# Performance work log

Measured on AMD Instinct MI355X. Metric: run time of the kernel, lower is better.

Reference implementation:

```python
import jax, jax.numpy as jnp
import numpy as np

KH = KW = 9
STRIDE = 1
PAD = 4
DIL = 1


def _bilinear(img, py, px):
    """img: [C,H,W]; py, px: [kk,Ho,Wo] float sample coords -> [C,kk,Ho,Wo].
    Zero padding outside the image, matching DCNv2 semantics."""
    H, W = img.shape[-2], img.shape[-1]
    y0 = jnp.floor(py)
    x0 = jnp.floor(px)
    wy = py - y0  # fractional parts (carry the gradient wrt offsets)
    wx = px - x0

    def gather(yi, xi):
        valid = ((yi >= 0) & (yi < H) & (xi >= 0) & (xi < W)).astype(img.dtype)
        yc = jnp.clip(yi, 0, H - 1).astype(jnp.int32)
        xc = jnp.clip(xi, 0, W - 1).astype(jnp.int32)
        return img[:, yc, xc] * valid[None]

    v00 = gather(y0, x0)
    v01 = gather(y0, x0 + 1)
    v10 = gather(y0 + 1, x0)
    v11 = gather(y0 + 1, x0 + 1)
    return (v00 * (1 - wy) * (1 - wx) + v01 * (1 - wy) * wx
            + v10 * wy * (1 - wx) + v11 * wy * wx)


def setup_inputs() -> dict:
    key = jax.random.key(0)
    k1, k2, k3 = jax.random.split(key, 3)
    B, H, W = 2, 256, 256
    kk = KH * KW
    inp = jax.random.normal(k1, (B, 3, H, W), dtype=jnp.float32)
    offset = jax.random.normal(k2, (B, 2 * kk, H, W), dtype=jnp.float32)
    mask = jax.random.uniform(k3, (B, kk, H, W), dtype=jnp.float32)
    weight = jnp.ones((1, 1, KH, KW), dtype=jnp.float32) / kk  # frozen averaging kernel
    bias = jnp.zeros((1,), dtype=jnp.float32)
    return {"input": inp, "offset": offset, "mask": mask, "weight": weight, "bias": bias}


def reference(input, offset, mask, weight, bias):
    B, C, H, W = input.shape  # C = 3 * Ci (R,G,B chunks sharing weight/offset/mask)
    kk = KH * KW
    Ho = (H + 2 * PAD - DIL * (KH - 1) - 1) // STRIDE + 1
    Wo = (W + 2 * PAD - DIL * (KW - 1) - 1) // STRIDE + 1

    ky = jnp.repeat(jnp.arange(KH), KW)  # [kk]
    kx = jnp.tile(jnp.arange(KW), KH)
    base_y = (jnp.arange(Ho) * STRIDE - PAD)[None, :, None] + (ky * DIL)[:, None, None]  # [kk,Ho,1]
    base_x = (jnp.arange(Wo) * STRIDE - PAD)[None, None, :] + (kx * DIL)[:, None, None]  # [kk,1,Wo]

    off = offset.reshape(B, kk, 2, Ho, Wo)  # channel c = 2*k + {0: dy, 1: dx}
    py = base_y[None].astype(offset.dtype) + off[:, :, 0]  # [B,kk,Ho,Wo]
    px = base_x[None].astype(offset.dtype) + off[:, :, 1]

    # bilinear-sampled, modulated im2col: [B, C, kk, Ho, Wo]
    samples = jax.vmap(_bilinear)(input, py, px)
    val = samples * mask[:, None]

    Co, Ci = weight.shape[0], weight.shape[1]
    G = C // Ci  # 3 color groups, identical weight applied to each
    val = val.reshape(B, G, Ci, kk, Ho, Wo)
    wk = weight.reshape(Co, Ci, kk)
    out = jnp.einsum('bgckhw,ock->bgohw', val, wk) + bias[None, None, :, None, None]
    return out.reshape(B, G * Co, Ho, Wo)
```

## Files before the change

### kernel.cpp

```cpp
#include <hip/hip_runtime.h>
#include <hip/hip_fp16.h>

#define HH 256
#define WW 256
#define KK 81
#define PLANE (HH * WW)
#define SLK 10
#define TR 21
#define TC 150
#define TAB (TR * TC)

__global__ __launch_bounds__(256) void pack_kernel(const float* __restrict__ in,
                                                   ushort4* __restrict__ img) {
    int idx = blockIdx.x * 256 + threadIdx.x;
    int b = idx >> 16;
    int pix = idx & 0xFFFF;
    const float* base = in + (size_t)b * 3 * PLANE + pix;
    _Float16 h0 = (_Float16)base[0];
    _Float16 h1 = (_Float16)base[PLANE];
    _Float16 h2 = (_Float16)base[2 * PLANE];
    ushort4 u;
    u.x = __builtin_bit_cast(unsigned short, h0);
    u.y = __builtin_bit_cast(unsigned short, h1);
    u.z = __builtin_bit_cast(unsigned short, h2);
    u.w = 0;
    img[idx] = u;
}

__device__ __forceinline__ void acc3(float w, unsigned int pa, unsigned int pb,
                                     float& ax, float& ay, float& az) {
    __half2 ha = __builtin_bit_cast(__half2, pa);
    __half2 hb = __builtin_bit_cast(__half2, pb);
    ax = fmaf(w, __low2float(ha), ax);
    ay = fmaf(w, __high2float(ha), ay);
    az = fmaf(w, __low2float(hb), az);
}

__global__ __launch_bounds__(128, 3) void dcn_kernel(
    const ushort4* __restrict__ img,
    const float* __restrict__ offset,
    const float* __restrict__ mask,
    const float* __restrict__ weight,
    const float* __restrict__ bias,
    float* __restrict__ out) {
    __shared__ uint2 tile[TAB];

    const int t = threadIdx.x;
    const int b = blockIdx.y;
    const int ho = blockIdx.x >> 1;
    const int xo = (blockIdx.x & 1) * 128;
    const int yb = ho - SLK;
    const ushort4* ib = img + (size_t)b * PLANE;

    for (int i = 0; i < 25; ++i) {
        int cid = t + i * 128;
        if (cid < TAB) {
            int r = cid / TC;
            int c = cid - r * TC;
            int iy = yb + r;
            int ix = xo - SLK + c;
            unsigned int pa = 0, pb = 0;
            if (((unsigned)iy < (unsigned)HH) & ((unsigned)ix < (unsigned)WW)) {
                ushort4 u = ib[iy * WW + ix];
                pa = (unsigned int)u.x | ((unsigned int)u.y << 16);
                pb = (unsigned int)u.z;
            }
            tile[cid] = make_uint2(pa, pb);
        }
    }
    __syncthreads();

    const float* orow = offset + (size_t)b * 2 * KK * PLANE + (size_t)ho * WW + xo;
    const float* mrow = mask + (size_t)b * KK * PLANE + (size_t)ho * WW + xo;

    const float wof = (float)t;
    float ax = 0.f, ay = 0.f, az = 0.f;
    bool escaped = false;

    for (int ky = 0; ky < 9; ++ky) {
        const int rshift = ky + (SLK - 4);
#pragma unroll
        for (int kxi = 0; kxi < 9; ++kxi) {
            const int k = ky * 9 + kxi;
            float dy = orow[(size_t)(2 * k) * PLANE + t];
            float dx = orow[(size_t)(2 * k + 1) * PLANE + t];
            float m = mrow[(size_t)k * PLANE + t];
            float wk = weight[k];

            float yf = floorf(dy);
            float wy = dy - yf;
            int r0 = (int)yf + rshift;

            float px = dx + wof;
            float xf = floorf(px);
            float wx = px - xf;
            int c0 = (int)xf + (kxi + (SLK - 4));

            bool ok = ((unsigned)r0 < (unsigned)(TR - 1)) &
                      ((unsigned)c0 < (unsigned)(TC - 1));
            escaped |= !ok;
            float mw = (ok ? m : 0.f) * wk;

            float w1y = wy * mw, w0y = mw - w1y;
            float u1 = 1.f - wx;
            float w00 = w0y * u1, w01 = w0y * wx;
            float w10 = w1y * u1, w11 = w1y * wx;

            int r0c = min(max(r0, 0), TR - 2);
            int c0c = min(max(c0, 0), TC - 2);
            const uint2* p = &tile[r0c * TC + c0c];
            uint2 q00 = p[0];
            uint2 q01 = p[1];
            uint2 q10 = p[TC];
            uint2 q11 = p[TC + 1];

            acc3(w00, q00.x, q00.y, ax, ay, az);
            acc3(w01, q01.x, q01.y, ax, ay, az);
            acc3(w10, q10.x, q10.y, ax, ay, az);
            acc3(w11, q11.x, q11.y, ax, ay, az);
        }
    }

    if (__builtin_expect(escaped, 0)) {
#pragma unroll 1
        for (int k = 0; k < KK; ++k) {
            int ky = k / 9;
            int kxi = k - ky * 9;
            float dy = orow[(size_t)(2 * k) * PLANE + t];
            float dx = orow[(size_t)(2 * k + 1) * PLANE + t];
            float m = mrow[(size_t)k * PLANE + t];

            float yf = floorf(dy);
            int r0 = (int)yf + ky + (SLK - 4);
            float px = dx + wof;
            float xf = floorf(px);
            int c0 = (int)xf + kxi + (SLK - 4);
            bool ok = ((unsigned)r0 < (unsigned)(TR - 1)) &
                      ((unsigned)c0 < (unsigned)(TC - 1));
            if (ok) continue;

            float wy = dy - yf;
            float wx = px - xf;
            int y0 = (int)yf + ho - 4 + ky;
            int x0 = (int)xf + xo + kxi - 4;
            int y1 = y0 + 1, x1 = x0 + 1;
            float mw = m * weight[k];
            float va0 = ((unsigned)y0 < (unsigned)HH) ? 1.f : 0.f;
            float va1 = ((unsigned)y1 < (unsigned)HH) ? 1.f : 0.f;
            float vb0 = ((unsigned)x0 < (unsigned)WW) ? 1.f : 0.f;
            float vb1 = ((unsigned)x1 < (unsigned)WW) ? 1.f : 0.f;
            float w1y = wy * mw, w0y = mw - w1y;
            float w00 = w0y * (1.f - wx) * va0 * vb0;
            float w01 = w0y * wx * va0 * vb1;
            float w10 = w1y * (1.f - wx) * va1 * vb0;
            float w11 = w1y * wx * va1 * vb1;
            int y0c = min(max(y0, 0), HH - 1);
            int y1c = min(max(y1, 0), HH - 1);
            int x0c = min(max(x0, 0), WW - 1);
            int x1c = min(max(x1, 0), WW - 1);
            ushort4 g00 = ib[y0c * WW + x0c];
            ushort4 g01 = ib[y0c * WW + x1c];
            ushort4 g10 = ib[y1c * WW + x0c];
            ushort4 g11 = ib[y1c * WW + x1c];
            acc3(w00, (unsigned int)g00.x | ((unsigned int)g00.y << 16), g00.z, ax, ay, az);
            acc3(w01, (unsigned int)g01.x | ((unsigned int)g01.y << 16), g01.z, ax, ay, az);
            acc3(w10, (unsigned int)g10.x | ((unsigned int)g10.y << 16), g10.z, ax, ay, az);
            acc3(w11, (unsigned int)g11.x | ((unsigned int)g11.y << 16), g11.z, ax, ay, az);
        }
    }

    float bs = bias[0];
    float* ob = out + (size_t)b * 3 * PLANE + (size_t)ho * WW + xo + t;
    ob[0] = ax + bs;
    ob[PLANE] = ay + bs;
    ob[2 * PLANE] = az + bs;
}

extern "C" void kernel_launch(void* const* d_in, const int* in_sizes, int n_in,
                              void* d_out, int out_size, void* d_ws, size_t ws_size,
                              hipStream_t stream) {
    const float* input = (const float*)d_in[0];
    const float* offset = (const float*)d_in[1];
    const float* mask = (const float*)d_in[2];
    const float* weight = (const float*)d_in[3];
    const float* bias = (const float*)d_in[4];
    float* out = (float*)d_out;

    const int B = in_sizes[0] / (3 * PLANE);
    ushort4* img = (ushort4*)d_ws;

    pack_kernel<<<B * PLANE / 256, 256, 0, stream>>>(input, img);
    dim3 grid(HH * 2, B);
    dcn_kernel<<<grid, 128, 0, stream>>>(img, offset, mask, weight, bias, out);
}
```

Before: 172.8 us.

## Stream offset/mask rows into LDS ring via async global_load_lds prefetch

Result: slower. 192.7 us (+11.5%).

```diff
diff --git a/kernel.cpp b/kernel.cpp
--- a/kernel.cpp
+++ b/kernel.cpp
@@ -9,6 +9,7 @@
 #define TR 21
 #define TC 150
 #define TAB (TR * TC)
+#define RD 8
 
 __global__ __launch_bounds__(256) void pack_kernel(const float* __restrict__ in,
                                                    ushort4* __restrict__ img) {
@@ -36,7 +37,14 @@
     az = fmaf(w, __low2float(hb), az);
 }
 
-__global__ __launch_bounds__(128, 3) void dcn_kernel(
+__device__ __forceinline__ void gload_lds4(const float* g, float* l) {
+    __builtin_amdgcn_global_load_lds(
+        (const __attribute__((address_space(1))) unsigned int*)g,
+        (__attribute__((address_space(3))) unsigned int*)l,
+        4, 0, 0);
+}
+
+__global__ __launch_bounds__(128, 2) void dcn_kernel(
     const ushort4* __restrict__ img,
     const float* __restrict__ offset,
     const float* __restrict__ mask,
@@ -44,13 +52,30 @@
     const float* __restrict__ bias,
     float* __restrict__ out) {
     __shared__ uint2 tile[TAB];
+    __shared__ float ring[2][RD][192];
+    __shared__ float wk[KK];
 
     const int t = threadIdx.x;
+    const int wv = t >> 6;
+    const int l = t & 63;
     const int b = blockIdx.y;
     const int ho = blockIdx.x >> 1;
     const int xo = (blockIdx.x & 1) * 128;
     const int yb = ho - SLK;
     const ushort4* ib = img + (size_t)b * PLANE;
+
+    if (t < KK) wk[t] = weight[t];
+
+    const float* orow = offset + (size_t)b * 2 * KK * PLANE + (size_t)ho * WW + xo + wv * 64;
+    const float* mrow = mask + (size_t)b * KK * PLANE + (size_t)ho * WW + xo + wv * 64;
+
+#pragma unroll
+    for (int j = 0; j < RD; ++j) {
+        float* slot = &ring[wv][j][0];
+        gload_lds4(orow + (size_t)(2 * j) * PLANE + l, slot);
+        gload_lds4(orow + (size_t)(2 * j + 1) * PLANE + l, slot + 64);
+        gload_lds4(mrow + (size_t)j * PLANE + l, slot + 128);
+    }
 
     for (int i = 0; i < 25; ++i) {
         int cid = t + i * 128;
@@ -70,55 +95,109 @@
     }
     __syncthreads();
 
-    const float* orow = offset + (size_t)b * 2 * KK * PLANE + (size_t)ho * WW + xo;
-    const float* mrow = mask + (size_t)b * KK * PLANE + (size_t)ho * WW + xo;
-
     const float wof = (float)t;
     float ax = 0.f, ay = 0.f, az = 0.f;
     bool escaped = false;
 
-    for (int ky = 0; ky < 9; ++ky) {
-        const int rshift = ky + (SLK - 4);
-#pragma unroll
-        for (int kxi = 0; kxi < 9; ++kxi) {
-            const int k = ky * 9 + kxi;
-            float dy = orow[(size_t)(2 * k) * PLANE + t];
-            float dx = orow[(size_t)(2 * k + 1) * PLANE + t];
-            float m = mrow[(size_t)k * PLANE + t];
-            float wk = weight[k];
-
-            float yf = floorf(dy);
-            float wy = dy - yf;
-            int r0 = (int)yf + rshift;
-
-            float px = dx + wof;
-            float xf = floorf(px);
-            float wx = px - xf;
-            int c0 = (int)xf + (kxi + (SLK - 4));
-
-            bool ok = ((unsigned)r0 < (unsigned)(TR - 1)) &
-                      ((unsigned)c0 < (unsigned)(TC - 1));
-            escaped |= !ok;
-            float mw = (ok ? m : 0.f) * wk;
-
-            float w1y = wy * mw, w0y = mw - w1y;
-            float u1 = 1.f - wx;
-            float w00 = w0y * u1, w01 = w0y * wx;
-            float w10 = w1y * u1, w11 = w1y * wx;
-
-            int r0c = min(max(r0, 0), TR - 2);
-            int c0c = min(max(c0, 0), TC - 2);
-            const uint2* p = &tile[r0c * TC + c0c];
-            uint2 q00 = p[0];
-            uint2 q01 = p[1];
-            uint2 q10 = p[TC];
-            uint2 q11 = p[TC + 1];
-
-            acc3(w00, q00.x, q00.y, ax, ay, az);
-            acc3(w01, q01.x, q01.y, ax, ay, az);
-            acc3(w10, q10.x, q10.y, ax, ay, az);
-            acc3(w11, q11.x, q11.y, ax, ay, az);
+#pragma unroll 1
+    for (int j = 0; j < 73; ++j) {
+        asm volatile("s_waitcnt vmcnt(21)" ::: "memory");
+        __builtin_amdgcn_sched_barrier(0);
+
+        const float* slot = &ring[wv][j & (RD - 1)][0];
+        float dy = slot[l];
+        float dx = slot[64 + l];
+        float m = slot[128 + l];
+        float wkv = wk[j];
+        asm volatile("s_waitcnt lgkmcnt(0)" ::: "memory");
+        __builtin_amdgcn_sched_barrier(0);
+
+        {
+            float* ns = &ring[wv][j & (RD - 1)][0];
+            gload_lds4(orow + (size_t)(2 * (j + RD)) * PLANE + l, ns);
+            gload_lds4(orow + (size_t)(2 * (j + RD) + 1) * PLANE + l, ns + 64);
+            gload_lds4(mrow + (size_t)(j + RD) * PLANE + l, ns + 128);
         }
+
+        const int ky = j / 9;
+        const int kxi = j - ky * 9;
+
+        float yf = floorf(dy);
+        float wy = dy - yf;
+        int r0 = (int)yf + ky + (SLK - 4);
+
+        float px = dx + wof;
+        float xf = floorf(px);
+        float wx = px - xf;
+        int c0 = (int)xf + kxi + (SLK - 4);
+
+        bool ok = ((unsigned)r0 < (unsigned)(TR - 1)) &
+                  ((unsigned)c0 < (unsigned)(TC - 1));
+        escaped |= !ok;
+        float mw = (ok ? m : 0.f) * wkv;
+
+        float w1y = wy * mw, w0y = mw - w1y;
+        float u1 = 1.f - wx;
+        float w00 = w0y * u1, w01 = w0y * wx;
+        float w10 = w1y * u1, w11 = w1y * wx;
+
+        int r0c = min(max(r0, 0), TR - 2);
+        int c0c = min(max(c0, 0), TC - 2);
+        const uint2* p = &tile[r0c * TC + c0c];
+        uint2 q00 = p[0];
+        uint2 q01 = p[1];
+        uint2 q10 = p[TC];
+        uint2 q11 = p[TC + 1];
+
+        acc3(w00, q00.x, q00.y, ax, ay, az);
+        acc3(w01, q01.x, q01.y, ax, ay, az);
+        acc3(w10, q10.x, q10.y, ax, ay, az);
+        acc3(w11, q11.x, q11.y, ax, ay, az);
+    }
+
+    asm volatile("s_waitcnt vmcnt(0)" ::: "memory");
+    __builtin_amdgcn_sched_barrier(0);
+#pragma unroll 1
+    for (int j = 73; j < KK; ++j) {
+        const float* slot = &ring[wv][j & (RD - 1)][0];
+        float dy = slot[l];
+        float dx = slot[64 + l];
+        float m = slot[128 + l];
+        float wkv = wk[j];
+
+        const int ky = j / 9;
+        const int kxi = j - ky * 9;
+
+        float yf = floorf(dy);
+        float wy = dy - yf;
+        int r0 = (int)yf + ky + (SLK - 4);
+        float px = dx + wof;
+        float xf = floorf(px);
+        float wx = px - xf;
+        int c0 = (int)xf + kxi + (SLK - 4);
+
+        bool ok = ((unsigned)r0 < (unsigned)(TR - 1)) &
+                  ((unsigned)c0 < (unsigned)(TC - 1));
+        escaped |= !ok;
+        float mw = (ok ? m : 0.f) * wkv;
+
+        float w1y = wy * mw, w0y = mw - w1y;
+        float u1 = 1.f - wx;
+        float w00 = w0y * u1, w01 = w0y * wx;
+        float w10 = w1y * u1, w11 = w1y * wx;
+
+        int r0c = min(max(r0, 0), TR - 2);
+        int c0c = min(max(c0, 0), TC - 2);
+        const uint2* p = &tile[r0c * TC + c0c];
+        uint2 q00 = p[0];
+        uint2 q01 = p[1];
+        uint2 q10 = p[TC];
+        uint2 q11 = p[TC + 1];
+
+        acc3(w00, q00.x, q00.y, ax, ay, az);
+        acc3(w01, q01.x, q01.y, ax, ay, az);
+        acc3(w10, q10.x, q10.y, ax, ay, az);
+        acc3(w11, q11.x, q11.y, ax, ay, az);
     }
 
     if (__builtin_expect(escaped, 0)) {
@@ -126,9 +205,9 @@
         for (int k = 0; k < KK; ++k) {
             int ky = k / 9;
             int kxi = k - ky * 9;
-            float dy = orow[(size_t)(2 * k) * PLANE + t];
-            float dx = orow[(size_t)(2 * k + 1) * PLANE + t];
-            float m = mrow[(size_t)k * PLANE + t];
+            float dy = orow[(size_t)(2 * k) * PLANE + l];
+            float dx = orow[(size_t)(2 * k + 1) * PLANE + l];
+            float m = mrow[(size_t)k * PLANE + l];
 
             float yf = floorf(dy);
             int r0 = (int)yf + ky + (SLK - 4);
@@ -144,7 +223,7 @@
             int y0 = (int)yf + ho - 4 + ky;
             int x0 = (int)xf + xo + kxi - 4;
             int y1 = y0 + 1, x1 = x0 + 1;
-            float mw = m * weight[k];
+            float mw = m * wk[k];
             float va0 = ((unsigned)y0 < (unsigned)HH) ? 1.f : 0.f;
             float va1 = ((unsigned)y1 < (unsigned)HH) ? 1.f : 0.f;
             float vb0 = ((unsigned)x0 < (unsigned)WW) ? 1.f : 0.f;
```

## Replace LDS tile with direct global gathers and split taps across waves

Applied to the files above, without the earlier changes.

After: 193.6 us. 1.12x slower.

```diff
diff --git a/kernel.cpp b/kernel.cpp
--- a/kernel.cpp
+++ b/kernel.cpp
@@ -5,10 +5,6 @@
 #define WW 256
 #define KK 81
 #define PLANE (HH * WW)
-#define SLK 10
-#define TR 21
-#define TC 150
-#define TAB (TR * TC)
 
 __global__ __launch_bounds__(256) void pack_kernel(const float* __restrict__ in,
                                                    ushort4* __restrict__ img) {
@@ -36,144 +32,101 @@
     az = fmaf(w, __low2float(hb), az);
 }
 
-__global__ __launch_bounds__(128, 3) void dcn_kernel(
+__global__ __launch_bounds__(128, 4) void dcn_kernel(
     const ushort4* __restrict__ img,
     const float* __restrict__ offset,
     const float* __restrict__ mask,
     const float* __restrict__ weight,
     const float* __restrict__ bias,
     float* __restrict__ out) {
-    __shared__ uint2 tile[TAB];
+    __shared__ float red[3][64];
 
     const int t = threadIdx.x;
+    const int wv = t >> 6;
+    const int l = t & 63;
+    const int bx = blockIdx.x;
     const int b = blockIdx.y;
-    const int ho = blockIdx.x >> 1;
-    const int xo = (blockIdx.x & 1) * 128;
-    const int yb = ho - SLK;
-    const ushort4* ib = img + (size_t)b * PLANE;
+    const int ho = bx >> 2;
+    const int xo = (bx & 3) * 64;
+    const uint2* ibq = (const uint2*)img + (size_t)b * PLANE;
 
-    for (int i = 0; i < 25; ++i) {
-        int cid = t + i * 128;
-        if (cid < TAB) {
-            int r = cid / TC;
-            int c = cid - r * TC;
-            int iy = yb + r;
-            int ix = xo - SLK + c;
-            unsigned int pa = 0, pb = 0;
-            if (((unsigned)iy < (unsigned)HH) & ((unsigned)ix < (unsigned)WW)) {
-                ushort4 u = ib[iy * WW + ix];
-                pa = (unsigned int)u.x | ((unsigned int)u.y << 16);
-                pb = (unsigned int)u.z;
-            }
-            tile[cid] = make_uint2(pa, pb);
-        }
-    }
-    __syncthreads();
+    const int kb = wv * 41;
+    const int nk = 41 - wv;
 
-    const float* orow = offset + (size_t)b * 2 * KK * PLANE + (size_t)ho * WW + xo;
-    const float* mrow = mask + (size_t)b * KK * PLANE + (size_t)ho * WW + xo;
+    const float* orow = offset + (size_t)b * 2 * KK * PLANE + (size_t)(2 * kb) * PLANE
+                        + (size_t)ho * WW + xo;
+    const float* mrow = mask + (size_t)b * KK * PLANE + (size_t)kb * PLANE
+                        + (size_t)ho * WW + xo;
 
-    const float wof = (float)t;
+    const int wo = xo + l;
     float ax = 0.f, ay = 0.f, az = 0.f;
-    bool escaped = false;
 
-    for (int ky = 0; ky < 9; ++ky) {
-        const int rshift = ky + (SLK - 4);
-#pragma unroll
-        for (int kxi = 0; kxi < 9; ++kxi) {
-            const int k = ky * 9 + kxi;
-            float dy = orow[(size_t)(2 * k) * PLANE + t];
-            float dx = orow[(size_t)(2 * k + 1) * PLANE + t];
-            float m = mrow[(size_t)k * PLANE + t];
-            float wk = weight[k];
+    int ky = (kb == 41) ? 4 : 0;
+    int kxi = (kb == 41) ? 5 : 0;
 
-            float yf = floorf(dy);
-            float wy = dy - yf;
-            int r0 = (int)yf + rshift;
+#pragma unroll 4
+    for (int j = 0; j < nk; ++j) {
+        const int k = kb + j;
+        float dy = orow[(size_t)(2 * j) * PLANE + l];
+        float dx = orow[(size_t)(2 * j + 1) * PLANE + l];
+        float m = mrow[(size_t)j * PLANE + l];
+        float wkv = weight[k];
 
-            float px = dx + wof;
-            float xf = floorf(px);
-            float wx = px - xf;
-            int c0 = (int)xf + (kxi + (SLK - 4));
+        float yf = floorf(dy);
+        float wy = dy - yf;
+        int y0 = (int)yf + (ho - 4 + ky);
+        float fx = dx + (float)(kxi - 4);
+        float xf = floorf(fx);
+        float wx = fx - xf;
+        int x0 = (int)xf + wo;
+        int y1 = y0 + 1, x1 = x0 + 1;
 
-            bool ok = ((unsigned)r0 < (unsigned)(TR - 1)) &
-                      ((unsigned)c0 < (unsigned)(TC - 1));
-            escaped |= !ok;
-            float mw = (ok ? m : 0.f) * wk;
+        float va0 = ((unsigned)y0 < (unsigned)HH) ? 1.f : 0.f;
+        float va1 = ((unsigned)y1 < (unsigned)HH) ? 1.f : 0.f;
+        float vb0 = ((unsigned)x0 < (unsigned)WW) ? 1.f : 0.f;
+        float vb1 = ((unsigned)x1 < (unsigned)WW) ? 1.f : 0.f;
+        int y0c = min(max(y0, 0), HH - 1);
+        int y1c = min(max(y1, 0), HH - 1);
+        int x0c = min(max(x0, 0), WW - 1);
+        int x1c = min(max(x1, 0), WW - 1);
 
-            float w1y = wy * mw, w0y = mw - w1y;
-            float u1 = 1.f - wx;
-            float w00 = w0y * u1, w01 = w0y * wx;
-            float w10 = w1y * u1, w11 = w1y * wx;
+        float mw = m * wkv;
+        float w1y = wy * mw, w0y = mw - w1y;
+        float u1 = 1.f - wx;
+        float w00 = w0y * u1 * va0 * vb0;
+        float w01 = w0y * wx * va0 * vb1;
+        float w10 = w1y * u1 * va1 * vb0;
+        float w11 = w1y * wx * va1 * vb1;
 
-            int r0c = min(max(r0, 0), TR - 2);
-            int c0c = min(max(c0, 0), TC - 2);
-            const uint2* p = &tile[r0c * TC + c0c];
-            uint2 q00 = p[0];
-            uint2 q01 = p[1];
-            uint2 q10 = p[TC];
-            uint2 q11 = p[TC + 1];
+        uint2 q00 = ibq[y0c * WW + x0c];
+        uint2 q01 = ibq[y0c * WW + x1c];
+        uint2 q10 = ibq[y1c * WW + x0c];
+        uint2 q11 = ibq[y1c * WW + x1c];
 
-            acc3(w00, q00.x, q00.y, ax, ay, az);
-            acc3(w01, q01.x, q01.y, ax, ay, az);
-            acc3(w10, q10.x, q10.y, ax, ay, az);
-            acc3(w11, q11.x, q11.y, ax, ay, az);
+        acc3(w00, q00.x, q00.y, ax, ay, az);
+        acc3(w01, q01.x, q01.y, ax, ay, az);
+        acc3(w10, q10.x, q10.y, ax, ay, az);
+        acc3(w11, q11.x, q11.y, ax, ay, az);
+
+        if (++kxi == 9) {
+            kxi = 0;
+            ++ky;
         }
     }
 
-    if (__builtin_expect(escaped, 0)) {
-#pragma unroll 1
-        for (int k = 0; k < KK; ++k) {
-            int ky = k / 9;
-            int kxi = k - ky * 9;
-            float dy = orow[(size_t)(2 * k) * PLANE + t];
-            float dx = orow[(size_t)(2 * k + 1) * PLANE + t];
-            float m = mrow[(size_t)k * PLANE + t];
-
-            float yf = floorf(dy);
-            int r0 = (int)yf + ky + (SLK - 4);
-            float px = dx + wof;
-            float xf = floorf(px);
-            int c0 = (int)xf + kxi + (SLK - 4);
-            bool ok = ((unsigned)r0 < (unsigned)(TR - 1)) &
-                      ((unsigned)c0 < (unsigned)(TC - 1));
-            if (ok) continue;
-
-            float wy = dy - yf;
-            float wx = px - xf;
-            int y0 = (int)yf + ho - 4 + ky;
-            int x0 = (int)xf + xo + kxi - 4;
-            int y1 = y0 + 1, x1 = x0 + 1;
-            float mw = m * weight[k];
-            float va0 = ((unsigned)y0 < (unsigned)HH) ? 1.f : 0.f;
-            float va1 = ((unsigned)y1 < (unsigned)HH) ? 1.f : 0.f;
-            float vb0 = ((unsigned)x0 < (unsigned)WW) ? 1.f : 0.f;
-            float vb1 = ((unsigned)x1 < (unsigned)WW) ? 1.f : 0.f;
-            float w1y = wy * mw, w0y = mw - w1y;
-            float w00 = w0y * (1.f - wx) * va0 * vb0;
-            float w01 = w0y * wx * va0 * vb1;
-            float w10 = w1y * (1.f - wx) * va1 * vb0;
-            float w11 = w1y * wx * va1 * vb1;
-            int y0c = min(max(y0, 0), HH - 1);
-            int y1c = min(max(y1, 0), HH - 1);
-            int x0c = min(max(x0, 0), WW - 1);
-            int x1c = min(max(x1, 0), WW - 1);
-            ushort4 g00 = ib[y0c * WW + x0c];
-            ushort4 g01 = ib[y0c * WW + x1c];
-            ushort4 g10 = ib[y1c * WW + x0c];
-            ushort4 g11 = ib[y1c * WW + x1c];
-            acc3(w00, (unsigned int)g00.x | ((unsigned int)g00.y << 16), g00.z, ax, ay, az);
-            acc3(w01, (unsigned int)g01.x | ((unsigned int)g01.y << 16), g01.z, ax, ay, az);
-            acc3(w10, (unsigned int)g10.x | ((unsigned int)g10.y << 16), g10.z, ax, ay, az);
-            acc3(w11, (unsigned int)g11.x | ((unsigned int)g11.y << 16), g11.z, ax, ay, az);
-        }
+    if (wv == 1) {
+        red[0][l] = ax;
+        red[1][l] = ay;
+        red[2][l] = az;
     }
-
-    float bs = bias[0];
-    float* ob = out + (size_t)b * 3 * PLANE + (size_t)ho * WW + xo + t;
-    ob[0] = ax + bs;
-    ob[PLANE] = ay + bs;
-    ob[2 * PLANE] = az + bs;
+    __syncthreads();
+    if (wv == 0) {
+        float bs = bias[0];
+        float* ob = out + (size_t)b * 3 * PLANE + (size_t)ho * WW + xo + l;
+        ob[0] = ax + red[0][l] + bs;
+        ob[PLANE] = ay + red[1][l] + bs;
+        ob[2 * PLANE] = az + red[2][l] + bs;
+    }
 }
 
 extern "C" void kernel_launch(void* const* d_in, const int* in_sizes, int n_in,
@@ -190,6 +143,6 @@
     ushort4* img = (ushort4*)d_ws;
 
     pack_kernel<<<B * PLANE / 256, 256, 0, stream>>>(input, img);
-    dim3 grid(HH * 2, B);
+    dim3 grid(HH * 4, B);
     dcn_kernel<<<grid, 128, 0, stream>>>(img, offset, mask, weight, bias, out);
 }
```

## Split kernel taps across waves with 4 pixels per lane and LDS reduction

Applied to the files above, without the earlier changes.

After: 171.5 us. No clear change (-0.8%).

```diff
diff --git a/kernel.cpp b/kernel.cpp
--- a/kernel.cpp
+++ b/kernel.cpp
@@ -7,8 +7,8 @@
 #define PLANE (HH * WW)
 #define SLK 10
 #define TR 21
-#define TC 150
-#define TAB (TR * TC)
+#define TCW 276
+#define TABW (TR * TCW)
 
 __global__ __launch_bounds__(256) void pack_kernel(const float* __restrict__ in,
                                                    ushort4* __restrict__ img) {
@@ -36,29 +36,31 @@
     az = fmaf(w, __low2float(hb), az);
 }
 
-__global__ __launch_bounds__(128, 3) void dcn_kernel(
+__global__ __launch_bounds__(256) void dcn_kernel(
     const ushort4* __restrict__ img,
     const float* __restrict__ offset,
     const float* __restrict__ mask,
     const float* __restrict__ weight,
     const float* __restrict__ bias,
     float* __restrict__ out) {
-    __shared__ uint2 tile[TAB];
+    __shared__ uint2 tile[TABW];
+    __shared__ float red[3][4][256];
 
     const int t = threadIdx.x;
+    const int w = t >> 6;
+    const int l = t & 63;
     const int b = blockIdx.y;
-    const int ho = blockIdx.x >> 1;
-    const int xo = (blockIdx.x & 1) * 128;
+    const int ho = blockIdx.x;
     const int yb = ho - SLK;
     const ushort4* ib = img + (size_t)b * PLANE;
 
-    for (int i = 0; i < 25; ++i) {
-        int cid = t + i * 128;
-        if (cid < TAB) {
-            int r = cid / TC;
-            int c = cid - r * TC;
+    for (int i = 0; i < 23; ++i) {
+        int cid = t + i * 256;
+        if (cid < TABW) {
+            int r = cid / TCW;
+            int c = cid - r * TCW;
             int iy = yb + r;
-            int ix = xo - SLK + c;
+            int ix = c - SLK;
             unsigned int pa = 0, pb = 0;
             if (((unsigned)iy < (unsigned)HH) & ((unsigned)ix < (unsigned)WW)) {
                 ushort4 u = ib[iy * WW + ix];
@@ -70,36 +72,49 @@
     }
     __syncthreads();
 
-    const float* orow = offset + (size_t)b * 2 * KK * PLANE + (size_t)ho * WW + xo;
-    const float* mrow = mask + (size_t)b * KK * PLANE + (size_t)ho * WW + xo;
-
-    const float wof = (float)t;
-    float ax = 0.f, ay = 0.f, az = 0.f;
-    bool escaped = false;
-
-    for (int ky = 0; ky < 9; ++ky) {
-        const int rshift = ky + (SLK - 4);
+    const int kbeg = w * 20 + (w ? 1 : 0);
+    const int nk = w ? 20 : 21;
+    int ky = kbeg / 9;
+    int kxi = kbeg - ky * 9;
+
+    const float* obase = offset + (size_t)b * 2 * KK * PLANE
+                         + (size_t)(2 * kbeg) * PLANE + (size_t)ho * WW;
+    const float* mbase = mask + (size_t)b * KK * PLANE
+                         + (size_t)kbeg * PLANE + (size_t)ho * WW;
+
+    float ax[4] = {0.f, 0.f, 0.f, 0.f};
+    float ay[4] = {0.f, 0.f, 0.f, 0.f};
+    float az[4] = {0.f, 0.f, 0.f, 0.f};
+    bool esc = false;
+
+#pragma unroll 2
+    for (int j = 0; j < nk; ++j) {
+        float4 dy4 = *(const float4*)(obase + (size_t)(2 * j) * PLANE + 4 * l);
+        float4 dx4 = *(const float4*)(obase + (size_t)(2 * j + 1) * PLANE + 4 * l);
+        float4 m4 = *(const float4*)(mbase + (size_t)j * PLANE + 4 * l);
+        float wkv = weight[kbeg + j];
+
+        const float dyv[4] = {dy4.x, dy4.y, dy4.z, dy4.w};
+        const float dxv[4] = {dx4.x, dx4.y, dx4.z, dx4.w};
+        const float mv[4] = {m4.x, m4.y, m4.z, m4.w};
+
 #pragma unroll
-        for (int kxi = 0; kxi < 9; ++kxi) {
-            const int k = ky * 9 + kxi;
-            float dy = orow[(size_t)(2 * k) * PLANE + t];
-            float dx = orow[(size_t)(2 * k + 1) * PLANE + t];
-            float m = mrow[(size_t)k * PLANE + t];
-            float wk = weight[k];
-
+        for (int i = 0; i < 4; ++i) {
+            const int wo = 4 * l + i;
+            float dy = dyv[i];
             float yf = floorf(dy);
             float wy = dy - yf;
-            int r0 = (int)yf + rshift;
-
-            float px = dx + wof;
-            float xf = floorf(px);
-            float wx = px - xf;
-            int c0 = (int)xf + (kxi + (SLK - 4));
+            int r0 = (int)yf + ky + (SLK - 4);
+
+            float fx = dxv[i] + (float)(kxi - 4);
+            float xf = floorf(fx);
+            float wx = fx - xf;
+            int c0 = (int)xf + wo + SLK;
 
             bool ok = ((unsigned)r0 < (unsigned)(TR - 1)) &
-                      ((unsigned)c0 < (unsigned)(TC - 1));
-            escaped |= !ok;
-            float mw = (ok ? m : 0.f) * wk;
+                      ((unsigned)c0 < (unsigned)(TCW - 1));
+            esc |= !ok;
+            float mw = (ok ? mv[i] : 0.f) * wkv;
 
             float w1y = wy * mw, w0y = mw - w1y;
             float u1 = 1.f - wx;
@@ -107,73 +122,100 @@
             float w10 = w1y * u1, w11 = w1y * wx;
 
             int r0c = min(max(r0, 0), TR - 2);
-            int c0c = min(max(c0, 0), TC - 2);
-            const uint2* p = &tile[r0c * TC + c0c];
+            int c0c = min(max(c0, 0), TCW - 2);
+            const uint2* p = &tile[r0c * TCW + c0c];
             uint2 q00 = p[0];
             uint2 q01 = p[1];
-            uint2 q10 = p[TC];
-            uint2 q11 = p[TC + 1];
-
-            acc3(w00, q00.x, q00.y, ax, ay, az);
-            acc3(w01, q01.x, q01.y, ax, ay, az);
-            acc3(w10, q10.x, q10.y, ax, ay, az);
-            acc3(w11, q11.x, q11.y, ax, ay, az);
-        }
-    }
-
-    if (__builtin_expect(escaped, 0)) {
+            uint2 q10 = p[TCW];
+            uint2 q11 = p[TCW + 1];
+
+            acc3(w00, q00.x, q00.y, ax[i], ay[i], az[i]);
+            acc3(w01, q01.x, q01.y, ax[i], ay[i], az[i]);
+            acc3(w10, q10.x, q10.y, ax[i], ay[i], az[i]);
+            acc3(w11, q11.x, q11.y, ax[i], ay[i], az[i]);
+        }
+
+        if (++kxi == 9) {
+            kxi = 0;
+            ++ky;
+        }
+    }
+
+    if (__builtin_expect(esc, 0)) {
 #pragma unroll 1
-        for (int k = 0; k < KK; ++k) {
-            int ky = k / 9;
-            int kxi = k - ky * 9;
-            float dy = orow[(size_t)(2 * k) * PLANE + t];
-            float dx = orow[(size_t)(2 * k + 1) * PLANE + t];
-            float m = mrow[(size_t)k * PLANE + t];
-
-            float yf = floorf(dy);
-            int r0 = (int)yf + ky + (SLK - 4);
-            float px = dx + wof;
-            float xf = floorf(px);
-            int c0 = (int)xf + kxi + (SLK - 4);
-            bool ok = ((unsigned)r0 < (unsigned)(TR - 1)) &
-                      ((unsigned)c0 < (unsigned)(TC - 1));
-            if (ok) continue;
-
-            float wy = dy - yf;
-            float wx = px - xf;
-            int y0 = (int)yf + ho - 4 + ky;
-            int x0 = (int)xf + xo + kxi - 4;
-            int y1 = y0 + 1, x1 = x0 + 1;
-            float mw = m * weight[k];
-            float va0 = ((unsigned)y0 < (unsigned)HH) ? 1.f : 0.f;
-            float va1 = ((unsigned)y1 < (unsigned)HH) ? 1.f : 0.f;
-            float vb0 = ((unsigned)x0 < (unsigned)WW) ? 1.f : 0.f;
-            float vb1 = ((unsigned)x1 < (unsigned)WW) ? 1.f : 0.f;
-            float w1y = wy * mw, w0y = mw - w1y;
-            float w00 = w0y * (1.f - wx) * va0 * vb0;
-            float w01 = w0y * wx * va0 * vb1;
-            float w10 = w1y * (1.f - wx) * va1 * vb0;
-            float w11 = w1y * wx * va1 * vb1;
-            int y0c = min(max(y0, 0), HH - 1);
-            int y1c = min(max(y1, 0), HH - 1);
-            int x0c = min(max(x0, 0), WW - 1);
-            int x1c = min(max(x1, 0), WW - 1);
-            ushort4 g00 = ib[y0c * WW + x0c];
-            ushort4 g01 = ib[y0c * WW + x1c];
-            ushort4 g10 = ib[y1c * WW + x0c];
-            ushort4 g11 = ib[y1c * WW + x1c];
-            acc3(w00, (unsigned int)g00.x | ((unsigned int)g00.y << 16), g00.z, ax, ay, az);
-            acc3(w01, (unsigned int)g01.x | ((unsigned int)g01.y << 16), g01.z, ax, ay, az);
-            acc3(w10, (unsigned int)g10.x | ((unsigned int)g10.y << 16), g10.z, ax, ay, az);
-            acc3(w11, (unsigned int)g11.x | ((unsigned int)g11.y << 16), g11.z, ax, ay, az);
-        }
-    }
-
-    float bs = bias[0];
-    float* ob = out + (size_t)b * 3 * PLANE + (size_t)ho * WW + xo + t;
-    ob[0] = ax + bs;
-    ob[PLANE] = ay + bs;
-    ob[2 * PLANE] = az + bs;
+        for (int j = 0; j < nk; ++j) {
+            int k = kbeg + j;
+            int kyy = k / 9;
+            int kxx = k - kyy * 9;
+#pragma unroll
+            for (int i = 0; i < 4; ++i) {
+                const int wo = 4 * l + i;
+                float dy = obase[(size_t)(2 * j) * PLANE + wo];
+                float dx = obase[(size_t)(2 * j + 1) * PLANE + wo];
+                float m = mbase[(size_t)j * PLANE + wo];
+
+                float yf = floorf(dy);
+                int r0 = (int)yf + kyy + (SLK - 4);
+                float fx = dx + (float)(kxx - 4);
+                float xf = floorf(fx);
+                int c0 = (int)xf + wo + SLK;
+                bool ok = ((unsigned)r0 < (unsigned)(TR - 1)) &
+                          ((unsigned)c0 < (unsigned)(TCW - 1));
+                if (ok) continue;
+
+                float wy = dy - yf;
+                float wx = fx - xf;
+                int y0 = (int)yf + ho - 4 + kyy;
+                int x0 = (int)xf + wo + kxx - 4;
+                int y1 = y0 + 1, x1 = x0 + 1;
+                float mw = m * weight[k];
+                float va0 = ((unsigned)y0 < (unsigned)HH) ? 1.f : 0.f;
+                float va1 = ((unsigned)y1 < (unsigned)HH) ? 1.f : 0.f;
+                float vb0 = ((unsigned)x0 < (unsigned)WW) ? 1.f : 0.f;
+                float vb1 = ((unsigned)x1 < (unsigned)WW) ? 1.f : 0.f;
+                float w1y = wy * mw, w0y = mw - w1y;
+                float w00 = w0y * (1.f - wx) * va0 * vb0;
+                float w01 = w0y * wx * va0 * vb1;
+                float w10 = w1y * (1.f - wx) * va1 * vb0;
+                float w11 = w1y * wx * va1 * vb1;
+                int y0c = min(max(y0, 0), HH - 1);
+                int y1c = min(max(y1, 0), HH - 1);
+                int x0c = min(max(x0, 0), WW - 1);
+                int x1c = min(max(x1, 0), WW - 1);
+                ushort4 g00 = ib[y0c * WW + x0c];
+                ushort4 g01 = ib[y0c * WW + x1c];
+                ushort4 g10 = ib[y1c * WW + x0c];
+                ushort4 g11 = ib[y1c * WW + x1c];
+                acc3(w00, (unsigned int)g00.x | ((unsigned int)g00.y << 16), g00.z,
+                     ax[i], ay[i], az[i]);
+                acc3(w01, (unsigned int)g01.x | ((unsigned int)g01.y << 16), g01.z,
+                     ax[i], ay[i], az[i]);
+                acc3(w10, (unsigned int)g10.x | ((unsigned int)g10.y << 16), g10.z,
+                     ax[i], ay[i], az[i]);
+                acc3(w11, (unsigned int)g11.x | ((unsigned int)g11.y << 16), g11.z,
+                     ax[i], ay[i], az[i]);
+            }
+        }
+    }
+
+#pragma unroll
+    for (int i = 0; i < 4; ++i) {
+        red[0][w][4 * l + i] = ax[i];
+        red[1][w][4 * l + i] = ay[i];
+        red[2][w][4 * l + i] = az[i];
+    }
+    __syncthreads();
+
+    {
+        float bs = bias[0];
+        float* ob = out + (size_t)b * 3 * PLANE + (size_t)ho * WW + t;
+        float s0 = red[0][0][t] + red[0][1][t] + red[0][2][t] + red[0][3][t];
+        float s1 = red[1][0][t] + red[1][1][t] + red[1][2][t] + red[1][3][t];
+        float s2 = red[2][0][t] + red[2][1][t] + red[2][2][t] + red[2][3][t];
+        ob[0] = s0 + bs;
+        ob[PLANE] = s1 + bs;
+        ob[2 * PLANE] = s2 + bs;
+    }
 }
 
 extern "C" void kernel_launch(void* const* d_in, const int* in_sizes, int n_in,
@@ -190,6 +232,6 @@
     ushort4* img = (ushort4*)d_ws;
 
     pack_kernel<<<B * PLANE / 256, 256, 0, stream>>>(input, img);
-    dim3 grid(HH * 2, B);
-    dcn_kernel<<<grid, 128, 0, stream>>>(img, offset, mask, weight, bias, out);
-}
+    dim3 grid(HH, B);
+    dcn_kernel<<<grid, 256, 0, stream>>>(img, offset, mask, weight, bias, out);
+}
```
